# Kernel optimization log

Measured on AMD Instinct MI355X. Metric: run time of the kernel, lower is better.

## Reference

```python
import jax, jax.numpy as jnp
import numpy as np

B = 128
H = 512
S_TOK = 512
S_DESC = 128
N_NODES = 65536
MARGIN = 0.05
COS_EPS = 1e-8


def setup_inputs() -> dict:
    key = jax.random.key(0)
    ks = jax.random.split(key, 26)
    sc = 1.0 / np.sqrt(H)
    inp = {
        "token_feat": jax.random.normal(ks[0], (B, S_TOK, H), jnp.float32),
        "token_len": jnp.maximum(jax.random.randint(ks[1], (B,), 0, S_TOK), 1),
        "node_h": jax.random.normal(ks[2], (N_NODES, H), jnp.float32),
        "seg_ids": jnp.sort(jax.random.randint(ks[3], (N_NODES,), 0, B)),
        "desc_anchor_feat": jax.random.normal(ks[4], (B, S_DESC, H), jnp.float32),
        "desc_anchor_len": jnp.maximum(jax.random.randint(ks[5], (B,), 0, S_DESC), 1),
        "desc_neg_feat": jax.random.normal(ks[6], (B, S_DESC, H), jnp.float32),
        "desc_neg_len": jnp.maximum(jax.random.randint(ks[7], (B,), 0, S_DESC), 1),
        # attention params: Linear(H,H) weight/bias, Linear(H,1) weight/bias
        "Wt": jax.random.normal(ks[8], (H, H), jnp.float32) * sc,
        "bt": jax.random.normal(ks[9], (H,), jnp.float32) * sc,
        "vt": jax.random.normal(ks[10], (H,), jnp.float32) * sc,
        "ct": jax.random.normal(ks[11], (), jnp.float32) * sc,
        "Wa": jax.random.normal(ks[12], (H, H), jnp.float32) * sc,
        "ba": jax.random.normal(ks[13], (H,), jnp.float32) * sc,
        "va": jax.random.normal(ks[14], (H,), jnp.float32) * sc,
        "ca": jax.random.normal(ks[15], (), jnp.float32) * sc,
        "Wd": jax.random.normal(ks[16], (H, H), jnp.float32) * sc,
        "bd": jax.random.normal(ks[17], (H,), jnp.float32) * sc,
        "vd": jax.random.normal(ks[18], (H,), jnp.float32) * sc,
        "cd": jax.random.normal(ks[19], (), jnp.float32) * sc,
        "Wf": jax.random.normal(ks[20], (2 * H, H), jnp.float32) * sc,
        "bf": jax.random.normal(ks[21], (H,), jnp.float32) * sc,
    }
    return inp


def masked_attn_pool(feat, lens, W, b, v, c):
    # feat: [B,S,H]; lens: [B]. Masked softmax attention pooling == the
    # per-sample masked_select + softmax + bmm loop, vectorized.
    logits = jnp.einsum("bsh,h->bs", jnp.tanh(jnp.einsum("bsh,hk->bsk", feat, W) + b), v) + c
    mask = jnp.arange(feat.shape[1])[None, :] < lens[:, None]
    logits = jnp.where(mask, logits, -jnp.inf)
    w = jax.nn.softmax(logits, axis=1)  # [B,S]
    return jnp.einsum("bs,bsh->bh", w, feat)


def segment_attn_pool(h, seg, W, b, v, c, num_segments):
    # h: [N,H] packed node states; seg: [N] sample id. Per-segment softmax attn
    # pooling == the per-sample slice + softmax + bmm loop over tree_node_num.
    logits = jnp.tanh(h @ W + b) @ v + c  # [N]
    m = jax.ops.segment_max(logits, seg, num_segments=num_segments)
    e = jnp.exp(logits - m[seg])
    denom = jax.ops.segment_sum(e, seg, num_segments=num_segments)
    w = e / denom[seg]
    return jax.ops.segment_sum(w[:, None] * h, seg, num_segments=num_segments)


def cosine_sim(a, b):
    na = jnp.maximum(jnp.linalg.norm(a, axis=1), COS_EPS)
    nb = jnp.maximum(jnp.linalg.norm(b, axis=1), COS_EPS)
    return jnp.sum(a * b, axis=1) / (na * nb)


def reference(token_feat, token_len, node_h, seg_ids, desc_anchor_feat,
              desc_anchor_len, desc_neg_feat, desc_neg_len,
              Wt, bt, vt, ct, Wa, ba, va, ca, Wd, bd, vd, cd, Wf, bf):
    # token modality (use_token_attn, then use_tanh)
    tok = jnp.tanh(masked_attn_pool(token_feat, token_len, Wt, bt, vt, ct))
    # AST modality: use_tanh applies to node states BEFORE attention
    hn = jnp.tanh(node_h)
    ast = jnp.tanh(segment_attn_pool(hn, seg_ids, Wa, ba, va, ca, B))
    code_feat = jnp.tanh(jnp.concatenate([tok, ast], axis=1) @ Wf + bf)
    # desc modality: attn pool, use_tanh, then the extra unconditional tanh
    da = jnp.tanh(jnp.tanh(masked_attn_pool(desc_anchor_feat, desc_anchor_len, Wd, bd, vd, cd)))
    dn = jnp.tanh(jnp.tanh(masked_attn_pool(desc_neg_feat, desc_neg_len, Wd, bd, vd, cd)))
    anchor_sim = cosine_sim(code_feat, da)
    neg_sim = cosine_sim(code_feat, dn)
    loss = jnp.mean(jnp.maximum(MARGIN - anchor_sim + neg_sim, 1e-6))
    return loss
```

## Files before the change

kernel.cpp:

```cpp
#include <hip/hip_runtime.h>
#include <math.h>

#define HDIM 512
#define BATCH 128

typedef _Float16 f16x8 __attribute__((ext_vector_type(8)));
typedef float f32x4 __attribute__((ext_vector_type(4)));

__device__ __forceinline__ float fast_tanh(float x) {
  float e = __expf(2.0f * x);
  return 1.0f - 2.0f / (e + 1.0f);
}

__device__ __forceinline__ void gload_lds16(const void* g, void* l) {
  __builtin_amdgcn_global_load_lds(
      (const __attribute__((address_space(1))) unsigned int*)g,
      (__attribute__((address_space(3))) unsigned int*)l, 16, 0, 0);
}

__global__ __launch_bounds__(256) void cvt_all_kernel(
    const float* __restrict__ tok, const float* __restrict__ node,
    const float* __restrict__ da, const float* __restrict__ dn,
    _Float16* __restrict__ A2tok, _Float16* __restrict__ A2node,
    _Float16* __restrict__ A2desc) {
  const int seg = blockIdx.y;
  const float* A;
  _Float16* A2;
  int Mtot, m_off, Mrows;
  bool do_tanh = false;
  if (seg == 0)      { A = tok;  A2 = A2tok;  Mtot = 65536; m_off = 0;     Mrows = 65536; }
  else if (seg == 1) { A = node; A2 = A2node; Mtot = 65536; m_off = 0;     Mrows = 65536; do_tanh = true; }
  else if (seg == 2) { A = da;   A2 = A2desc; Mtot = 32768; m_off = 0;     Mrows = 16384; }
  else               { A = dn;   A2 = A2desc; Mtot = 32768; m_off = 16384; Mrows = 16384; }
  const int total = Mrows * 64;
  for (int i = blockIdx.x * 256 + threadIdx.x; i < total; i += gridDim.x * 256) {
    const int m = i >> 6, c = i & 63;
    const int kt = c >> 3, cc = c & 7;
    const float* src = A + (size_t)m * HDIM + c * 8;
    const float4 x = ((const float4*)src)[0];
    const float4 y = ((const float4*)src)[1];
    f16x8 h;
    if (do_tanh) {
      h[0] = (_Float16)fast_tanh(x.x); h[1] = (_Float16)fast_tanh(x.y);
      h[2] = (_Float16)fast_tanh(x.z); h[3] = (_Float16)fast_tanh(x.w);
      h[4] = (_Float16)fast_tanh(y.x); h[5] = (_Float16)fast_tanh(y.y);
      h[6] = (_Float16)fast_tanh(y.z); h[7] = (_Float16)fast_tanh(y.w);
    } else {
      h[0] = (_Float16)x.x; h[1] = (_Float16)x.y;
      h[2] = (_Float16)x.z; h[3] = (_Float16)x.w;
      h[4] = (_Float16)y.x; h[5] = (_Float16)y.y;
      h[6] = (_Float16)y.z; h[7] = (_Float16)y.w;
    }
    const int dr = m_off + m;
    char* dst = (char*)A2 + ((size_t)kt * Mtot + dr) * 128 + ((cc * 16) ^ ((dr & 7) << 4));
    *(f16x8*)dst = h;
  }
}

__global__ __launch_bounds__(256) void cvt_w3_kernel(
    const float* __restrict__ Wt, const float* __restrict__ Wa,
    const float* __restrict__ Wd, _Float16* __restrict__ W2t,
    _Float16* __restrict__ W2a, _Float16* __restrict__ W2d) {
  const int i = blockIdx.x * 256 + threadIdx.x;
  if (i >= 512 * 64) return;
  const float* W = (blockIdx.y == 0) ? Wt : (blockIdx.y == 1) ? Wa : Wd;
  _Float16* W2 = (blockIdx.y == 0) ? W2t : (blockIdx.y == 1) ? W2a : W2d;
  const int n = i & 511, g = i >> 9;
  const int kt = g >> 3, cc = g & 7;
  f16x8 h;
#pragma unroll
  for (int j = 0; j < 8; ++j)
    h[j] = (_Float16)W[(size_t)(kt * 64 + cc * 8 + j) * HDIM + n];
  char* dst = (char*)W2 + ((size_t)kt * 512 + n) * 128 + ((cc * 16) ^ ((n & 7) << 4));
  *(f16x8*)dst = h;
}

__global__ __launch_bounds__(512, 1) void gemm_logits_m_kernel(
    const _Float16* __restrict__ A2tok, const _Float16* __restrict__ A2node,
    const _Float16* __restrict__ A2desc,
    const _Float16* __restrict__ W2t, const _Float16* __restrict__ W2a,
    const _Float16* __restrict__ W2d,
    const float* __restrict__ bt, const float* __restrict__ vt,
    const float* __restrict__ ba, const float* __restrict__ va,
    const float* __restrict__ bd, const float* __restrict__ vd,
    float* __restrict__ logits_tok, float* __restrict__ logits_node,
    float* __restrict__ logits_desc) {
  __shared__ __align__(16) _Float16 As[2][256 * 64];
  __shared__ __align__(16) _Float16 Bs[2][256 * 64];

  const int tid = threadIdx.x;
  const int nwg = gridDim.x;
  const int qq = nwg >> 3;
  const int raw = (int)blockIdx.x;
  const int swz = (raw & 7) * qq + (raw >> 3);

  int id, local;
  if (swz < 512)       { id = 0; local = swz; }
  else if (swz < 1024) { id = 1; local = swz - 512; }
  else                 { id = 2; local = swz - 1024; }
  const int mb = local >> 1, nb = local & 1;
  const _Float16* A2 = (id == 0) ? A2tok : (id == 1) ? A2node : A2desc;
  const _Float16* W2 = (id == 0) ? W2t : (id == 1) ? W2a : W2d;
  const float* bias = (id == 0) ? bt : (id == 1) ? ba : bd;
  const float* vvec = (id == 0) ? vt : (id == 1) ? va : vd;
  float* logits = (id == 0) ? logits_tok : (id == 1) ? logits_node : logits_desc;
  const int M = (id == 2) ? 32768 : 65536;
  const size_t m0 = (size_t)mb * 256;
  const int n0 = nb * 256;

  const int lane = tid & 63, wid = tid >> 6;
  const int tx = lane & 15, qd = lane >> 4;
  const int wm = wid >> 2;
  const int wn = wid & 3;

  const char* gA = (const char*)A2 + m0 * 128;
  const char* gB = (const char*)W2 + (size_t)n0 * 128;
  const size_t sA = (size_t)M * 128;
  const size_t sB = (size_t)512 * 128;
  const int lo = tid * 16;
  const int wlo = wid * 1024;

  f32x4 acc[8][4];
#pragma unroll
  for (int i = 0; i < 8; ++i)
#pragma unroll
    for (int j = 0; j < 4; ++j) acc[i][j] = (f32x4){0.f, 0.f, 0.f, 0.f};

  auto STAGE_A = [&](int buf, int kt) {
    const char* a = gA + (size_t)kt * sA;
#pragma unroll
    for (int p = 0; p < 4; ++p)
      gload_lds16(a + lo + p * 8192, (char*)As[buf] + wlo + p * 8192);
  };
  auto STAGE_B = [&](int buf, int kt) {
    const char* b = gB + (size_t)kt * sB;
#pragma unroll
    for (int p = 0; p < 4; ++p)
      gload_lds16(b + lo + p * 8192, (char*)Bs[buf] + wlo + p * 8192);
  };

  auto HALF = [&](int buf, int ks) {
    f16x8 aF[8], bF[4];
#pragma unroll
    for (int i = 0; i < 8; ++i) {
      const int row = wm * 128 + i * 16 + tx;
      int by = row * 128 + (ks * 32 + qd * 8) * 2;
      by ^= (row & 7) << 4;
      aF[i] = *(const f16x8*)((const char*)As[buf] + by);
    }
#pragma unroll
    for (int j = 0; j < 4; ++j) {
      const int n = wn * 64 + j * 16 + tx;
      int by = n * 128 + (ks * 32 + qd * 8) * 2;
      by ^= (n & 7) << 4;
      bF[j] = *(const f16x8*)((const char*)Bs[buf] + by);
    }
    __builtin_amdgcn_s_setprio(1);
#pragma unroll
    for (int i = 0; i < 8; ++i)
#pragma unroll
      for (int j = 0; j < 4; ++j)
        acc[i][j] = __builtin_amdgcn_mfma_f32_16x16x32_f16(aF[i], bF[j], acc[i][j], 0, 0, 0);
    __builtin_amdgcn_s_setprio(0);
  };

  STAGE_A(0, 0);
  STAGE_B(0, 0);
#pragma unroll
  for (int t = 0; t < 8; ++t) {
    const int cur = t & 1;
    if (t < 7) {
      STAGE_A(cur ^ 1, t + 1);
      asm volatile("s_waitcnt vmcnt(4)" ::: "memory");
    } else {
      asm volatile("s_waitcnt vmcnt(0)" ::: "memory");
    }
    __builtin_amdgcn_s_barrier();
    asm volatile("" ::: "memory");
    HALF(cur, 0);
    asm volatile("" ::: "memory");
    __builtin_amdgcn_s_barrier();
    asm volatile("" ::: "memory");
    if (t < 7) STAGE_B(cur ^ 1, t + 1);
    HALF(cur, 1);
    asm volatile("" ::: "memory");
    __builtin_amdgcn_s_barrier();
    asm volatile("" ::: "memory");
  }

  float vv[4], bb[4];
#pragma unroll
  for (int j = 0; j < 4; ++j) {
    const int n = n0 + wn * 64 + j * 16 + tx;
    vv[j] = vvec[n];
    bb[j] = bias[n];
  }
#pragma unroll
  for (int i = 0; i < 8; ++i) {
#pragma unroll
    for (int r = 0; r < 4; ++r) {
      float s = 0.0f;
#pragma unroll
      for (int j = 0; j < 4; ++j)
        s = fmaf(vv[j], fast_tanh(acc[i][j][r] + bb[j]), s);
      s += __shfl_xor(s, 1);
      s += __shfl_xor(s, 2);
      s += __shfl_xor(s, 4);
      s += __shfl_xor(s, 8);
      if (tx == 0)
        atomicAdd(&logits[m0 + wm * 128 + i * 16 + qd * 4 + r], s);
    }
  }
}


__global__ void zero_kernel(float* __restrict__ p, int n) {
  const int i = blockIdx.x * 256 + threadIdx.x;
  if (i < n) p[i] = 0.0f;
}

__global__ void seg_bounds_kernel(const int* __restrict__ seg, int N,
                                  int* __restrict__ seg_start) {
  const int b = threadIdx.x;
  if (b > BATCH) return;
  int lo = 0, hi = N;
  while (lo < hi) {
    const int mid = (lo + hi) >> 1;
    if (seg[mid] < b) lo = mid + 1; else hi = mid;
  }
  seg_start[b] = lo;
}

__global__ __launch_bounds__(256) void softmax_all_kernel(
    float* __restrict__ ltok, float* __restrict__ ldesc,
    float* __restrict__ lnode, const int* __restrict__ tlen,
    const int* __restrict__ dalen, const int* __restrict__ dnlen,
    const int* __restrict__ seg_start) {
  __shared__ float smax[4], ssum[4];
  const int b = blockIdx.x, mode = blockIdx.y, tid = threadIdx.x;
  float* l;
  int s0, s1, fill_end;
  if (mode == 0)      { l = ltok + (size_t)b * 512;          s0 = 0; s1 = tlen[b];  fill_end = 512; }
  else if (mode == 1) { l = ldesc + (size_t)b * 128;         s0 = 0; s1 = dalen[b]; fill_end = 128; }
  else if (mode == 2) { l = ldesc + 16384 + (size_t)b * 128; s0 = 0; s1 = dnlen[b]; fill_end = 128; }
  else                { l = lnode; s0 = seg_start[b]; s1 = seg_start[b + 1]; fill_end = -1; }

  float mymax = -1e30f;
  for (int s = s0 + tid; s < s1; s += 256) mymax = fmaxf(mymax, l[s]);
#pragma unroll
  for (int off = 32; off; off >>= 1) mymax = fmaxf(mymax, __shfl_xor(mymax, off));
  if ((tid & 63) == 0) smax[tid >> 6] = mymax;
  __syncthreads();
  const float bmax = fmaxf(fmaxf(smax[0], smax[1]), fmaxf(smax[2], smax[3]));
  float mysum = 0.0f;
  for (int s = s0 + tid; s < s1; s += 256) mysum += __expf(l[s] - bmax);
#pragma unroll
  for (int off = 32; off; off >>= 1) mysum += __shfl_xor(mysum, off);
  if ((tid & 63) == 0) ssum[tid >> 6] = mysum;
  __syncthreads();
  const float inv = 1.0f / (ssum[0] + ssum[1] + ssum[2] + ssum[3]);
  for (int s = s0 + tid; s < s1; s += 256) l[s] = __expf(l[s] - bmax) * inv;
  if (fill_end > 0)
    for (int s = s1 + tid; s < fill_end; s += 256) l[s] = 0.0f;
}

__global__ __launch_bounds__(256) void pool_masked_all_kernel(
    const _Float16* __restrict__ A2tok, const _Float16* __restrict__ A2desc,
    const float* __restrict__ ltok, const float* __restrict__ ldesc,
    float* __restrict__ tok_pool, float* __restrict__ da_pool,
    float* __restrict__ dn_pool) {
  const int b = blockIdx.x, c = blockIdx.y, tid = threadIdx.x;
  const _Float16* A2;
  const float* w;
  float* out;
  int Mtot, rbase, s0;
  if (c < 8)       { A2 = A2tok;  Mtot = 65536; rbase = b * 512;         w = ltok;  out = tok_pool; s0 = c * 64; }
  else if (c < 10) { A2 = A2desc; Mtot = 32768; rbase = b * 128;         w = ldesc; out = da_pool;  s0 = (c - 8) * 64; }
  else             { A2 = A2desc; Mtot = 32768; rbase = 16384 + b * 128; w = ldesc; out = dn_pool;  s0 = (c - 10) * 64; }
  const int h = tid * 2;
  const int kt = h >> 6, col = h & 63;
  const char* base = (const char*)A2 + (size_t)kt * Mtot * 128;
  float ax = 0.0f, ay = 0.0f;
  for (int s = s0; s < s0 + 64; ++s) {
    const int row = rbase + s;
    const float wsc = w[row];
    if (wsc != 0.0f) {
      const unsigned u = *(const unsigned*)(base + (size_t)row * 128 + ((col * 2) ^ ((row & 7) << 4)));
      const _Float16* hp = (const _Float16*)&u;
      ax = fmaf(wsc, (float)hp[0], ax);
      ay = fmaf(wsc, (float)hp[1], ay);
    }
  }
  atomicAdd(&out[b * HDIM + h], ax);
  atomicAdd(&out[b * HDIM + h + 1], ay);
}

__global__ __launch_bounds__(256) void pool_tiled_seg_kernel(
    const _Float16* __restrict__ A2, const float* __restrict__ w,
    const int* __restrict__ seg_start, float* __restrict__ pool, int Mtot) {
  const int b = blockIdx.x, c = blockIdx.y, tid = threadIdx.x;
  const int h = tid * 2;
  const int kt = h >> 6, col = h & 63;
  const char* base = (const char*)A2 + (size_t)kt * Mtot * 128;
  const int s0 = seg_start[b], s1 = seg_start[b + 1];
  const int nseg = s1 - s0;
  const int chunk = (nseg + (int)gridDim.y - 1) / (int)gridDim.y;
  const int a0 = s0 + c * chunk;
  const int a1 = min(s1, a0 + chunk);
  float ax = 0.0f, ay = 0.0f;
  for (int s = a0; s < a1; ++s) {
    const float wsc = w[s];
    const unsigned u = *(const unsigned*)(base + (size_t)s * 128 + ((col * 2) ^ ((s & 7) << 4)));
    const _Float16* hp = (const _Float16*)&u;
    ax = fmaf(wsc, (float)hp[0], ax);
    ay = fmaf(wsc, (float)hp[1], ay);
  }
  atomicAdd(&pool[b * HDIM + h], ax);
  atomicAdd(&pool[b * HDIM + h + 1], ay);
}

__global__ __launch_bounds__(256) void code_gemm_kernel(
    const float* __restrict__ tok_pool, const float* __restrict__ ast_pool,
    const float* __restrict__ Wf, float* __restrict__ parts) {
  __shared__ float catS[128][65];
  __shared__ float4 wfS[64][32];
  const int nb = blockIdx.x, kb = blockIdx.y, tid = threadIdx.x;
  const int k0 = kb * 64;
  const float* src = (k0 < 512) ? (tok_pool + k0) : (ast_pool + (k0 - 512));
  for (int i = tid; i < 128 * 16; i += 256) {
    const int r = i >> 4, c4 = i & 15;
    const float4 v = *(const float4*)(src + (size_t)r * HDIM + c4 * 4);
    catS[r][c4 * 4 + 0] = fast_tanh(v.x);
    catS[r][c4 * 4 + 1] = fast_tanh(v.y);
    catS[r][c4 * 4 + 2] = fast_tanh(v.z);
    catS[r][c4 * 4 + 3] = fast_tanh(v.w);
  }
  for (int i = tid; i < 64 * 32; i += 256) {
    const int r = i >> 5, c = i & 31;
    wfS[r][c] = *(const float4*)(Wf + (size_t)(k0 + r) * HDIM + nb * 128 + c * 4);
  }
  __syncthreads();
  const int tb = tid >> 4, tn = tid & 15;
  const int b0 = tb * 8, n0l = tn * 8;
  float acc[8][8];
#pragma unroll
  for (int i = 0; i < 8; ++i)
#pragma unroll
    for (int j = 0; j < 8; ++j) acc[i][j] = 0.0f;
  for (int k = 0; k < 64; ++k) {
    float a[8];
#pragma unroll
    for (int i = 0; i < 8; ++i) a[i] = catS[b0 + i][k];
    const float4 w0 = wfS[k][tn * 2], w1 = wfS[k][tn * 2 + 1];
    const float wv[8] = {w0.x, w0.y, w0.z, w0.w, w1.x, w1.y, w1.z, w1.w};
#pragma unroll
    for (int i = 0; i < 8; ++i)
#pragma unroll
      for (int j = 0; j < 8; ++j) acc[i][j] = fmaf(a[i], wv[j], acc[i][j]);
  }
  float* dst = parts + ((size_t)kb * 128) * HDIM + nb * 128;
#pragma unroll
  for (int i = 0; i < 8; ++i) {
    const float4 o0 = {acc[i][0], acc[i][1], acc[i][2], acc[i][3]};
    const float4 o1 = {acc[i][4], acc[i][5], acc[i][6], acc[i][7]};
    *(float4*)(dst + (size_t)(b0 + i) * HDIM + n0l) = o0;
    *(float4*)(dst + (size_t)(b0 + i) * HDIM + n0l + 4) = o1;
  }
}

__global__ __launch_bounds__(256) void sims_kernel(
    const float* __restrict__ parts, const float* __restrict__ bfv,
    const float* __restrict__ da_pool, const float* __restrict__ dn_pool,
    float* __restrict__ terms) {
  __shared__ float sr[4][5];
  const int b = blockIdx.x, tid = threadIdx.x;
  float c2 = 0, a2 = 0, n2 = 0, ca = 0, cn = 0;
  for (int i = tid; i < HDIM; i += 256) {
    float pre = bfv[i];
#pragma unroll
    for (int kb = 0; kb < 16; ++kb)
      pre += parts[((size_t)kb * 128 + b) * HDIM + i];
    const float cf = fast_tanh(pre);
    const float av = fast_tanh(fast_tanh(da_pool[(size_t)b * HDIM + i]));
    const float nv = fast_tanh(fast_tanh(dn_pool[(size_t)b * HDIM + i]));
    c2 = fmaf(cf, cf, c2); a2 = fmaf(av, av, a2); n2 = fmaf(nv, nv, n2);
    ca = fmaf(cf, av, ca); cn = fmaf(cf, nv, cn);
  }
#pragma unroll
  for (int off = 32; off; off >>= 1) {
    c2 += __shfl_xor(c2, off); a2 += __shfl_xor(a2, off); n2 += __shfl_xor(n2, off);
    ca += __shfl_xor(ca, off); cn += __shfl_xor(cn, off);
  }
  const int wv = tid >> 6;
  if ((tid & 63) == 0) {
    sr[wv][0] = c2; sr[wv][1] = a2; sr[wv][2] = n2; sr[wv][3] = ca; sr[wv][4] = cn;
  }
  __syncthreads();
  if (tid == 0) {
    c2 = sr[0][0] + sr[1][0] + sr[2][0] + sr[3][0];
    a2 = sr[0][1] + sr[1][1] + sr[2][1] + sr[3][1];
    n2 = sr[0][2] + sr[1][2] + sr[2][2] + sr[3][2];
    ca = sr[0][3] + sr[1][3] + sr[2][3] + sr[3][3];
    cn = sr[0][4] + sr[1][4] + sr[2][4] + sr[3][4];
    const float nc = fmaxf(sqrtf(c2), 1e-8f);
    const float na = fmaxf(sqrtf(a2), 1e-8f);
    const float nn = fmaxf(sqrtf(n2), 1e-8f);
    terms[b] = fmaxf(0.05f - ca / (nc * na) + cn / (nc * nn), 1e-6f);
  }
}

__global__ void loss_kernel(const float* __restrict__ terms, float* __restrict__ out) {
  const int tid = threadIdx.x;
  float v = terms[tid];
#pragma unroll
  for (int off = 32; off; off >>= 1) v += __shfl_xor(v, off);
  __shared__ float sr[2];
  if ((tid & 63) == 0) sr[tid >> 6] = v;
  __syncthreads();
  if (tid == 0) out[0] = (sr[0] + sr[1]) * (1.0f / (float)BATCH);
}


extern "C" void kernel_launch(void* const* d_in, const int* in_sizes, int n_in,
                              void* d_out, int out_size, void* d_ws, size_t ws_size,
                              hipStream_t stream) {
  (void)in_sizes; (void)n_in; (void)out_size; (void)ws_size;
  const float* token_feat = (const float*)d_in[0];
  const int*   token_len  = (const int*)d_in[1];
  const float* node_h     = (const float*)d_in[2];
  const int*   seg_ids    = (const int*)d_in[3];
  const float* da_feat    = (const float*)d_in[4];
  const int*   da_len     = (const int*)d_in[5];
  const float* dn_feat    = (const float*)d_in[6];
  const int*   dn_len     = (const int*)d_in[7];
  const float* Wt = (const float*)d_in[8];
  const float* bt = (const float*)d_in[9];
  const float* vt = (const float*)d_in[10];
  const float* Wa = (const float*)d_in[12];
  const float* ba = (const float*)d_in[13];
  const float* va = (const float*)d_in[14];
  const float* Wd = (const float*)d_in[16];
  const float* bd = (const float*)d_in[17];
  const float* vd = (const float*)d_in[18];
  const float* Wf  = (const float*)d_in[20];
  const float* bfv = (const float*)d_in[21];

  const int MTOK = 65536;
  const int MDESC2 = 32768;
  const int NNODES = 65536;

  float* ws = (float*)d_ws;
  float* logits_tok  = ws;
  float* logits_node = logits_tok + MTOK;
  float* logits_desc = logits_node + NNODES;
  float* tok_pool    = logits_desc + MDESC2;
  float* ast_pool    = tok_pool + 128 * HDIM;
  float* da_pool     = ast_pool + 128 * HDIM;
  float* dn_pool     = da_pool + 128 * HDIM;
  float* terms       = dn_pool + 128 * HDIM;
  int*   seg_start   = (int*)(terms + 128);
  float* parts       = (float*)(seg_start + 256);
  _Float16* W2t = (_Float16*)(parts + 16 * 128 * HDIM);
  _Float16* W2a = W2t + HDIM * HDIM;
  _Float16* W2d = W2a + HDIM * HDIM;
  _Float16* A2tok  = W2d + HDIM * HDIM;
  _Float16* A2node = A2tok + (size_t)8 * MTOK * 64;
  _Float16* A2desc = A2node + (size_t)8 * NNODES * 64;

  const int ZTOT = MTOK + NNODES + MDESC2 + 4 * 128 * HDIM;
  zero_kernel<<<dim3((ZTOT + 255) / 256), 256, 0, stream>>>(ws, ZTOT);
  seg_bounds_kernel<<<1, 256, 0, stream>>>(seg_ids, NNODES, seg_start);

  cvt_w3_kernel<<<dim3(128, 3), 256, 0, stream>>>(Wt, Wa, Wd, W2t, W2a, W2d);
  cvt_all_kernel<<<dim3(2048, 4), 256, 0, stream>>>(
      token_feat, node_h, da_feat, dn_feat, A2tok, A2node, A2desc);

  gemm_logits_m_kernel<<<1280, 512, 0, stream>>>(
      A2tok, A2node, A2desc, W2t, W2a, W2d,
      bt, vt, ba, va, bd, vd, logits_tok, logits_node, logits_desc);

  softmax_all_kernel<<<dim3(BATCH, 4), 256, 0, stream>>>(
      logits_tok, logits_desc, logits_node, token_len, da_len, dn_len, seg_start);

  pool_masked_all_kernel<<<dim3(BATCH, 12), 256, 0, stream>>>(
      A2tok, A2desc, logits_tok, logits_desc, tok_pool, da_pool, dn_pool);
  pool_tiled_seg_kernel<<<dim3(BATCH, 4), 256, 0, stream>>>(
      A2node, logits_node, seg_start, ast_pool, NNODES);

  code_gemm_kernel<<<dim3(4, 16), 256, 0, stream>>>(tok_pool, ast_pool, Wf, parts);
  sims_kernel<<<BATCH, 256, 0, stream>>>(parts, bfv, da_pool, dn_pool, terms);
  loss_kernel<<<1, 128, 0, stream>>>(terms, (float*)d_out);
}
```

Baseline: 335.7 us.

## Pre-swizzle activations into MFMA fragment layout and load A directly to registers

After: 384.1 us. 1.14x slower.

```diff
diff --git a/kernel.cpp b/kernel.cpp
--- a/kernel.cpp
+++ b/kernel.cpp
@@ -17,6 +17,7 @@
       (const __attribute__((address_space(1))) unsigned int*)g,
       (__attribute__((address_space(3))) unsigned int*)l, 16, 0, 0);
 }
+
 
 __global__ __launch_bounds__(256) void cvt_all_kernel(
     const float* __restrict__ tok, const float* __restrict__ node,
@@ -26,16 +27,15 @@
   const int seg = blockIdx.y;
   const float* A;
   _Float16* A2;
-  int Mtot, m_off, Mrows;
+  int M16, m_off, Mrows;
   bool do_tanh = false;
-  if (seg == 0)      { A = tok;  A2 = A2tok;  Mtot = 65536; m_off = 0;     Mrows = 65536; }
-  else if (seg == 1) { A = node; A2 = A2node; Mtot = 65536; m_off = 0;     Mrows = 65536; do_tanh = true; }
-  else if (seg == 2) { A = da;   A2 = A2desc; Mtot = 32768; m_off = 0;     Mrows = 16384; }
-  else               { A = dn;   A2 = A2desc; Mtot = 32768; m_off = 16384; Mrows = 16384; }
+  if (seg == 0)      { A = tok;  A2 = A2tok;  M16 = 4096; m_off = 0;     Mrows = 65536; }
+  else if (seg == 1) { A = node; A2 = A2node; M16 = 4096; m_off = 0;     Mrows = 65536; do_tanh = true; }
+  else if (seg == 2) { A = da;   A2 = A2desc; M16 = 2048; m_off = 0;     Mrows = 16384; }
+  else               { A = dn;   A2 = A2desc; M16 = 2048; m_off = 16384; Mrows = 16384; }
   const int total = Mrows * 64;
   for (int i = blockIdx.x * 256 + threadIdx.x; i < total; i += gridDim.x * 256) {
     const int m = i >> 6, c = i & 63;
-    const int kt = c >> 3, cc = c & 7;
     const float* src = A + (size_t)m * HDIM + c * 8;
     const float4 x = ((const float4*)src)[0];
     const float4 y = ((const float4*)src)[1];
@@ -52,7 +52,9 @@
       h[6] = (_Float16)y.z; h[7] = (_Float16)y.w;
     }
     const int dr = m_off + m;
-    char* dst = (char*)A2 + ((size_t)kt * Mtot + dr) * 128 + ((cc * 16) ^ ((dr & 7) << 4));
+    const int frag = (c >> 3) * 2 + ((c >> 2) & 1);
+    const int lane = (dr & 15) + ((c & 3) << 4);
+    _Float16* dst = A2 + ((size_t)frag * M16 + (dr >> 4)) * 512 + lane * 8;
     *(f16x8*)dst = h;
   }
 }
@@ -75,7 +77,7 @@
   *(f16x8*)dst = h;
 }
 
-__global__ __launch_bounds__(512, 1) void gemm_logits_m_kernel(
+__global__ __launch_bounds__(256, 2) void gemm_logits_frag_kernel(
     const _Float16* __restrict__ A2tok, const _Float16* __restrict__ A2node,
     const _Float16* __restrict__ A2desc,
     const _Float16* __restrict__ W2t, const _Float16* __restrict__ W2a,
@@ -85,130 +87,121 @@
     const float* __restrict__ bd, const float* __restrict__ vd,
     float* __restrict__ logits_tok, float* __restrict__ logits_node,
     float* __restrict__ logits_desc) {
-  __shared__ __align__(16) _Float16 As[2][256 * 64];
   __shared__ __align__(16) _Float16 Bs[2][256 * 64];
 
   const int tid = threadIdx.x;
-  const int nwg = gridDim.x;
-  const int qq = nwg >> 3;
   const int raw = (int)blockIdx.x;
-  const int swz = (raw & 7) * qq + (raw >> 3);
+  const int swz = (raw & 7) * 320 + (raw >> 3);
 
   int id, local;
-  if (swz < 512)       { id = 0; local = swz; }
-  else if (swz < 1024) { id = 1; local = swz - 512; }
-  else                 { id = 2; local = swz - 1024; }
+  if (swz < 1024)      { id = 0; local = swz; }
+  else if (swz < 2048) { id = 1; local = swz - 1024; }
+  else                 { id = 2; local = swz - 2048; }
   const int mb = local >> 1, nb = local & 1;
   const _Float16* A2 = (id == 0) ? A2tok : (id == 1) ? A2node : A2desc;
   const _Float16* W2 = (id == 0) ? W2t : (id == 1) ? W2a : W2d;
   const float* bias = (id == 0) ? bt : (id == 1) ? ba : bd;
   const float* vvec = (id == 0) ? vt : (id == 1) ? va : vd;
   float* logits = (id == 0) ? logits_tok : (id == 1) ? logits_node : logits_desc;
-  const int M = (id == 2) ? 32768 : 65536;
-  const size_t m0 = (size_t)mb * 256;
+  const int M16 = (id == 2) ? 2048 : 4096;
+  const size_t m0 = (size_t)mb * 128;
   const int n0 = nb * 256;
 
   const int lane = tid & 63, wid = tid >> 6;
   const int tx = lane & 15, qd = lane >> 4;
-  const int wm = wid >> 2;
-  const int wn = wid & 3;
-
-  const char* gA = (const char*)A2 + m0 * 128;
+  const int wm = wid >> 1;
+  const int wn = wid & 1;
+
+  const _Float16* aBase = A2 + ((size_t)(m0 >> 4) + wm * 4) * 512 + lane * 8;
   const char* gB = (const char*)W2 + (size_t)n0 * 128;
-  const size_t sA = (size_t)M * 128;
-  const size_t sB = (size_t)512 * 128;
-  const int lo = tid * 16;
-  const int wlo = wid * 1024;
-
-  f32x4 acc[8][4];
-#pragma unroll
-  for (int i = 0; i < 8; ++i)
-#pragma unroll
-    for (int j = 0; j < 4; ++j) acc[i][j] = (f32x4){0.f, 0.f, 0.f, 0.f};
-
-  auto STAGE_A = [&](int buf, int kt) {
-    const char* a = gA + (size_t)kt * sA;
-#pragma unroll
-    for (int p = 0; p < 4; ++p)
-      gload_lds16(a + lo + p * 8192, (char*)As[buf] + wlo + p * 8192);
+
+  f32x4 acc[4][8];
+#pragma unroll
+  for (int i = 0; i < 4; ++i)
+#pragma unroll
+    for (int j = 0; j < 8; ++j) acc[i][j] = (f32x4){0.f, 0.f, 0.f, 0.f};
+
+  f16x8 aR[2][2][4];
+
+  auto LOAD_A = [&](int par, int kt) {
+#pragma unroll
+    for (int ks = 0; ks < 2; ++ks)
+#pragma unroll
+      for (int i = 0; i < 4; ++i)
+        aR[par][ks][i] =
+            *(const f16x8*)(aBase + ((size_t)(kt * 2 + ks) * M16 + i) * 512);
   };
   auto STAGE_B = [&](int buf, int kt) {
-    const char* b = gB + (size_t)kt * sB;
-#pragma unroll
-    for (int p = 0; p < 4; ++p)
-      gload_lds16(b + lo + p * 8192, (char*)Bs[buf] + wlo + p * 8192);
+    const char* b = gB + (size_t)kt * 65536;
+#pragma unroll
+    for (int p = 0; p < 8; ++p)
+      gload_lds16(b + tid * 16 + p * 4096, (char*)Bs[buf] + tid * 16 + p * 4096);
   };
-
-  auto HALF = [&](int buf, int ks) {
-    f16x8 aF[8], bF[4];
-#pragma unroll
-    for (int i = 0; i < 8; ++i) {
-      const int row = wm * 128 + i * 16 + tx;
-      int by = row * 128 + (ks * 32 + qd * 8) * 2;
-      by ^= (row & 7) << 4;
-      aF[i] = *(const f16x8*)((const char*)As[buf] + by);
+  auto COMPUTE = [&](int par, int buf) {
+#pragma unroll
+    for (int ks = 0; ks < 2; ++ks) {
+#pragma unroll
+      for (int half = 0; half < 2; ++half) {
+        f16x8 bF[4];
+#pragma unroll
+        for (int f = 0; f < 4; ++f) {
+          const int n = wn * 128 + (half * 4 + f) * 16 + tx;
+          int by = n * 128 + ((ks * 64 + qd * 16) ^ ((n & 7) << 4));
+          bF[f] = *(const f16x8*)((const char*)Bs[buf] + by);
+        }
+        __builtin_amdgcn_s_setprio(1);
+#pragma unroll
+        for (int i = 0; i < 4; ++i)
+#pragma unroll
+          for (int f = 0; f < 4; ++f)
+            acc[i][half * 4 + f] = __builtin_amdgcn_mfma_f32_16x16x32_f16(
+                aR[par][ks][i], bF[f], acc[i][half * 4 + f], 0, 0, 0);
+        __builtin_amdgcn_s_setprio(0);
+      }
     }
-#pragma unroll
-    for (int j = 0; j < 4; ++j) {
-      const int n = wn * 64 + j * 16 + tx;
-      int by = n * 128 + (ks * 32 + qd * 8) * 2;
-      by ^= (n & 7) << 4;
-      bF[j] = *(const f16x8*)((const char*)Bs[buf] + by);
-    }
-    __builtin_amdgcn_s_setprio(1);
-#pragma unroll
-    for (int i = 0; i < 8; ++i)
-#pragma unroll
-      for (int j = 0; j < 4; ++j)
-        acc[i][j] = __builtin_amdgcn_mfma_f32_16x16x32_f16(aF[i], bF[j], acc[i][j], 0, 0, 0);
-    __builtin_amdgcn_s_setprio(0);
   };
 
-  STAGE_A(0, 0);
+  LOAD_A(0, 0);
   STAGE_B(0, 0);
 #pragma unroll
   for (int t = 0; t < 8; ++t) {
     const int cur = t & 1;
     if (t < 7) {
-      STAGE_A(cur ^ 1, t + 1);
-      asm volatile("s_waitcnt vmcnt(4)" ::: "memory");
+      LOAD_A(cur ^ 1, t + 1);
+      STAGE_B(cur ^ 1, t + 1);
+      asm volatile("s_waitcnt vmcnt(16)" ::: "memory");
     } else {
       asm volatile("s_waitcnt vmcnt(0)" ::: "memory");
     }
     __builtin_amdgcn_s_barrier();
     asm volatile("" ::: "memory");
-    HALF(cur, 0);
+    COMPUTE(cur, cur);
     asm volatile("" ::: "memory");
     __builtin_amdgcn_s_barrier();
     asm volatile("" ::: "memory");
-    if (t < 7) STAGE_B(cur ^ 1, t + 1);
-    HALF(cur, 1);
-    asm volatile("" ::: "memory");
-    __builtin_amdgcn_s_barrier();
-    asm volatile("" ::: "memory");
-  }
-
-  float vv[4], bb[4];
-#pragma unroll
-  for (int j = 0; j < 4; ++j) {
-    const int n = n0 + wn * 64 + j * 16 + tx;
+  }
+
+  float vv[8], bb[8];
+#pragma unroll
+  for (int j = 0; j < 8; ++j) {
+    const int n = n0 + wn * 128 + j * 16 + tx;
     vv[j] = vvec[n];
     bb[j] = bias[n];
   }
 #pragma unroll
-  for (int i = 0; i < 8; ++i) {
+  for (int i = 0; i < 4; ++i) {
 #pragma unroll
     for (int r = 0; r < 4; ++r) {
       float s = 0.0f;
 #pragma unroll
-      for (int j = 0; j < 4; ++j)
+      for (int j = 0; j < 8; ++j)
         s = fmaf(vv[j], fast_tanh(acc[i][j][r] + bb[j]), s);
       s += __shfl_xor(s, 1);
       s += __shfl_xor(s, 2);
       s += __shfl_xor(s, 4);
       s += __shfl_xor(s, 8);
       if (tx == 0)
-        atomicAdd(&logits[m0 + wm * 128 + i * 16 + qd * 4 + r], s);
+        atomicAdd(&logits[m0 + wm * 64 + i * 16 + qd * 4 + r], s);
     }
   }
 }
@@ -264,6 +257,14 @@
     for (int s = s1 + tid; s < fill_end; s += 256) l[s] = 0.0f;
 }
 
+__device__ __forceinline__ unsigned frag_read2(
+    const _Float16* __restrict__ A2, int M16, int row, int h) {
+  const int frag = (h >> 6) * 2 + ((h >> 5) & 1);
+  const int lane = (row & 15) + (((h >> 3) & 3) << 4);
+  const size_t off = ((size_t)frag * M16 + (row >> 4)) * 512 + lane * 8 + (h & 7);
+  return *(const unsigned*)((const char*)A2 + off * 2);
+}
+
 __global__ __launch_bounds__(256) void pool_masked_all_kernel(
     const _Float16* __restrict__ A2tok, const _Float16* __restrict__ A2desc,
     const float* __restrict__ ltok, const float* __restrict__ ldesc,
@@ -273,19 +274,17 @@
   const _Float16* A2;
   const float* w;
   float* out;
-  int Mtot, rbase, s0;
-  if (c < 8)       { A2 = A2tok;  Mtot = 65536; rbase = b * 512;         w = ltok;  out = tok_pool; s0 = c * 64; }
-  else if (c < 10) { A2 = A2desc; Mtot = 32768; rbase = b * 128;         w = ldesc; out = da_pool;  s0 = (c - 8) * 64; }
-  else             { A2 = A2desc; Mtot = 32768; rbase = 16384 + b * 128; w = ldesc; out = dn_pool;  s0 = (c - 10) * 64; }
+  int M16, rbase, s0;
+  if (c < 8)       { A2 = A2tok;  M16 = 4096; rbase = b * 512;         w = ltok;  out = tok_pool; s0 = c * 64; }
+  else if (c < 10) { A2 = A2desc; M16 = 2048; rbase = b * 128;         w = ldesc; out = da_pool;  s0 = (c - 8) * 64; }
+  else             { A2 = A2desc; M16 = 2048; rbase = 16384 + b * 128; w = ldesc; out = dn_pool;  s0 = (c - 10) * 64; }
   const int h = tid * 2;
-  const int kt = h >> 6, col = h & 63;
-  const char* base = (const char*)A2 + (size_t)kt * Mtot * 128;
   float ax = 0.0f, ay = 0.0f;
   for (int s = s0; s < s0 + 64; ++s) {
     const int row = rbase + s;
     const float wsc = w[row];
     if (wsc != 0.0f) {
-      const unsigned u = *(const unsigned*)(base + (size_t)row * 128 + ((col * 2) ^ ((row & 7) << 4)));
+      const unsigned u = frag_read2(A2, M16, row, h);
       const _Float16* hp = (const _Float16*)&u;
       ax = fmaf(wsc, (float)hp[0], ax);
       ay = fmaf(wsc, (float)hp[1], ay);
@@ -297,11 +296,9 @@
 
 __global__ __launch_bounds__(256) void pool_tiled_seg_kernel(
     const _Float16* __restrict__ A2, const float* __restrict__ w,
-    const int* __restrict__ seg_start, float* __restrict__ pool, int Mtot) {
+    const int* __restrict__ seg_start, float* __restrict__ pool) {
   const int b = blockIdx.x, c = blockIdx.y, tid = threadIdx.x;
   const int h = tid * 2;
-  const int kt = h >> 6, col = h & 63;
-  const char* base = (const char*)A2 + (size_t)kt * Mtot * 128;
   const int s0 = seg_start[b], s1 = seg_start[b + 1];
   const int nseg = s1 - s0;
   const int chunk = (nseg + (int)gridDim.y - 1) / (int)gridDim.y;
@@ -310,7 +307,7 @@
   float ax = 0.0f, ay = 0.0f;
   for (int s = a0; s < a1; ++s) {
     const float wsc = w[s];
-    const unsigned u = *(const unsigned*)(base + (size_t)s * 128 + ((col * 2) ^ ((s & 7) << 4)));
+    const unsigned u = frag_read2(A2, 4096, s, h);
     const _Float16* hp = (const _Float16*)&u;
     ax = fmaf(wsc, (float)hp[0], ax);
     ay = fmaf(wsc, (float)hp[1], ay);
@@ -464,18 +461,18 @@
   _Float16* W2a = W2t + HDIM * HDIM;
   _Float16* W2d = W2a + HDIM * HDIM;
   _Float16* A2tok  = W2d + HDIM * HDIM;
-  _Float16* A2node = A2tok + (size_t)8 * MTOK * 64;
-  _Float16* A2desc = A2node + (size_t)8 * NNODES * 64;
+  _Float16* A2node = A2tok + (size_t)MTOK * 512;
+  _Float16* A2desc = A2node + (size_t)NNODES * 512;
 
   const int ZTOT = MTOK + NNODES + MDESC2 + 4 * 128 * HDIM;
   zero_kernel<<<dim3((ZTOT + 255) / 256), 256, 0, stream>>>(ws, ZTOT);
   seg_bounds_kernel<<<1, 256, 0, stream>>>(seg_ids, NNODES, seg_start);
 
   cvt_w3_kernel<<<dim3(128, 3), 256, 0, stream>>>(Wt, Wa, Wd, W2t, W2a, W2d);
-  cvt_all_kernel<<<dim3(2048, 4), 256, 0, stream>>>(
+  cvt_all_kernel<<<dim3(4096, 4), 256, 0, stream>>>(
       token_feat, node_h, da_feat, dn_feat, A2tok, A2node, A2desc);
 
-  gemm_logits_m_kernel<<<1280, 512, 0, stream>>>(
+  gemm_logits_frag_kernel<<<2560, 256, 0, stream>>>(
       A2tok, A2node, A2desc, W2t, W2a, W2d,
       bt, vt, ba, va, bd, vd, logits_tok, logits_node, logits_desc);
 
@@ -485,7 +482,7 @@
   pool_masked_all_kernel<<<dim3(BATCH, 12), 256, 0, stream>>>(
       A2tok, A2desc, logits_tok, logits_desc, tok_pool, da_pool, dn_pool);
   pool_tiled_seg_kernel<<<dim3(BATCH, 4), 256, 0, stream>>>(
-      A2node, logits_node, seg_start, ast_pool, NNODES);
+      A2node, logits_node, seg_start, ast_pool);
 
   code_gemm_kernel<<<dim3(4, 16), 256, 0, stream>>>(tok_pool, ast_pool, Wf, parts);
   sims_kernel<<<BATCH, 256, 0, stream>>>(parts, bfv, da_pool, dn_pool, terms);
```
